# Performance work log

Hardware: AMD Instinct MI355X
Metric: run time of the kernel (lower is better)

Reference implementation:

```python
import jax, jax.numpy as jnp
import numpy as np

B = 64        # graphs per batch
NPG = 512     # nodes per graph (batch = repeat(arange(B), NPG))
D = 128       # hidden_dim = input_dim
L = 3         # GCN layers
K = 16        # NTN tensors
BINS = 16     # histogram bins


def _prep_edges(ei, N, dtype):
    # GCNConv normalization: add self-loops, deg on targets, sym norm
    loop = jnp.arange(N)
    src = jnp.concatenate([ei[0], loop])
    dst = jnp.concatenate([ei[1], loop])
    deg = jnp.zeros((N,), dtype).at[dst].add(1.0)
    dinv = jnp.where(deg > 0, jax.lax.rsqrt(deg), 0.0)
    norm = (dinv[src] * dinv[dst])[:, None]
    return src, dst, norm


def _encode(x, src, dst, norm, gcn_w, gcn_b, bn_g, bn_b, bn_m, bn_v):
    # eval-mode BatchNorm (running stats), dropout = identity
    for l in range(L):
        h = x @ gcn_w[l].T                     # [N, D]
        x = jnp.zeros_like(h).at[dst].add(norm * h[src]) + gcn_b[l]
        x = (x - bn_m[l]) * jax.lax.rsqrt(bn_v[l] + 1e-5) * bn_g[l] + bn_b[l]
        x = jax.nn.relu(x)
    return x


def _attention_pool(emb, ctx_w, ctx_b, att_w, att_b):
    t = jnp.tanh(emb @ ctx_w.T + ctx_b)        # [N, D]
    s = (t @ att_w + att_b).reshape(B, NPG, 1)
    e = emb.reshape(B, NPG, D)
    w = jax.nn.softmax(s, axis=1)              # per-graph softmax
    return (w * e).sum(axis=1)                 # [B, D]


def _histogram(e1, e2):
    n1 = (e1 / jnp.maximum(jnp.linalg.norm(e1, axis=-1, keepdims=True), 1e-8)).reshape(B, NPG, D)
    n2 = (e2 / jnp.maximum(jnp.linalg.norm(e2, axis=-1, keepdims=True), 1e-8)).reshape(B, NPG, D)
    sims = jnp.einsum('bnd,bmd->bnm', n1, n2)  # [B, n, n] cosine sims in [-1,1]
    bi = jnp.clip(jnp.floor((sims + 1.0) * (BINS / 2.0)), 0, BINS - 1).astype(jnp.int32)
    flat = (jnp.arange(B, dtype=jnp.int32)[:, None] * BINS + bi.reshape(B, -1)).reshape(-1)
    hist = jax.ops.segment_sum(jnp.ones(flat.shape, jnp.float32), flat,
                               num_segments=B * BINS).reshape(B, BINS)
    return hist / (hist.sum(axis=1, keepdims=True) + 1e-8)


def _ntn(g1, g2, T, tb, w1, b1, w2, b2, w3, b3):
    tp = jnp.einsum('bd,kde,be->bk', g1, T, g2) + tb   # bilinear products
    h = jax.nn.relu(tp @ w1.T + b1)
    h = jax.nn.relu(h @ w2.T + b2)
    return jax.nn.sigmoid(h @ w3.T + b3)               # [B, 1]


def _forward(x1, x2, edge_index1, edge_index2,
             gcn_w, gcn_b, bn_gamma, bn_beta, bn_mean, bn_var,
             ctx_w, ctx_b, att_w, att_b,
             ntn_T, ntn_bias, ntn_w1, ntn_b1, ntn_w2, ntn_b2, ntn_w3, ntn_b3,
             hist_w1, hist_b1, hist_w2, hist_b2,
             fus_w1, fus_b1, fus_w2, fus_b2):
    N = x1.shape[0]
    s1, d1, n1 = _prep_edges(edge_index1, N, x1.dtype)
    s2, d2, n2 = _prep_edges(edge_index2, N, x2.dtype)
    e1 = _encode(x1, s1, d1, n1, gcn_w, gcn_b, bn_gamma, bn_beta, bn_mean, bn_var)
    e2 = _encode(x2, s2, d2, n2, gcn_w, gcn_b, bn_gamma, bn_beta, bn_mean, bn_var)
    g1 = _attention_pool(e1, ctx_w, ctx_b, att_w, att_b)
    g2 = _attention_pool(e2, ctx_w, ctx_b, att_w, att_b)
    ntn_sim = _ntn(g1, g2, ntn_T, ntn_bias, ntn_w1, ntn_b1, ntn_w2, ntn_b2, ntn_w3, ntn_b3)
    hist = _histogram(e1, e2)
    hemb = jax.nn.relu(hist @ hist_w1.T + hist_b1) @ hist_w2.T + hist_b2
    comb = jnp.concatenate([ntn_sim, hemb], axis=1)    # [B, 17]
    h = jax.nn.relu(comb @ fus_w1.T + fus_b1)
    return jax.nn.sigmoid(h @ fus_w2.T + fus_b2)       # [B, 1]


def setup_inputs() -> dict:
    key = jax.random.key(0)
    ks = jax.random.split(key, 32)
    N = B * NPG
    E = 16 * N
    sc = 0.05
    inp = {
        'x1': jax.random.normal(ks[0], (N, D), jnp.float32),
        'x2': jax.random.normal(ks[1], (N, D), jnp.float32),
        'edge_index1': jax.random.randint(ks[2], (2, E), 0, N),
        'edge_index2': jax.random.randint(ks[3], (2, E), 0, N),
        'batch1': jnp.repeat(jnp.arange(B), NPG),
        'batch2': jnp.repeat(jnp.arange(B), NPG),
        'gcn_w': jax.random.normal(ks[4], (L, D, D), jnp.float32) * sc,
        'gcn_b': jax.random.normal(ks[5], (L, D), jnp.float32) * sc,
        'bn_gamma': jnp.ones((L, D), jnp.float32),
        'bn_beta': jnp.zeros((L, D), jnp.float32),
        'bn_mean': jnp.zeros((L, D), jnp.float32),
        'bn_var': jnp.ones((L, D), jnp.float32),
        'ctx_w': jax.random.normal(ks[6], (D, D), jnp.float32) * sc,
        'ctx_b': jax.random.normal(ks[7], (D,), jnp.float32) * sc,
        'att_w': jax.random.normal(ks[8], (D,), jnp.float32) * sc,
        'att_b': jax.random.normal(ks[9], (1,), jnp.float32) * sc,
        'ntn_T': jax.random.normal(ks[10], (K, D, D), jnp.float32) * 0.02,
        'ntn_bias': jax.random.normal(ks[11], (K,), jnp.float32) * sc,
        'ntn_w1': jax.random.normal(ks[12], (32, K), jnp.float32) * 0.2,
        'ntn_b1': jax.random.normal(ks[13], (32,), jnp.float32) * sc,
        'ntn_w2': jax.random.normal(ks[14], (16, 32), jnp.float32) * 0.15,
        'ntn_b2': jax.random.normal(ks[15], (16,), jnp.float32) * sc,
        'ntn_w3': jax.random.normal(ks[16], (1, 16), jnp.float32) * 0.2,
        'ntn_b3': jax.random.normal(ks[17], (1,), jnp.float32) * sc,
        'hist_w1': jax.random.normal(ks[18], (32, BINS), jnp.float32) * 0.2,
        'hist_b1': jax.random.normal(ks[19], (32,), jnp.float32) * sc,
        'hist_w2': jax.random.normal(ks[20], (16, 32), jnp.float32) * 0.15,
        'hist_b2': jax.random.normal(ks[21], (16,), jnp.float32) * sc,
        'fus_w1': jax.random.normal(ks[22], (8, 17), jnp.float32) * 0.2,
        'fus_b1': jax.random.normal(ks[23], (8,), jnp.float32) * sc,
        'fus_w2': jax.random.normal(ks[24], (1, 8), jnp.float32) * 0.3,
        'fus_b2': jax.random.normal(ks[25], (1,), jnp.float32) * sc,
    }
    return inp


def reference(x1, x2, edge_index1, edge_index2, batch1, batch2,
              gcn_w, gcn_b, bn_gamma, bn_beta, bn_mean, bn_var,
              ctx_w, ctx_b, att_w, att_b,
              ntn_T, ntn_bias, ntn_w1, ntn_b1, ntn_w2, ntn_b2, ntn_w3, ntn_b3,
              hist_w1, hist_b1, hist_w2, hist_b2,
              fus_w1, fus_b1, fus_w2, fus_b2):
    # batch1/batch2 encode 64 equal-sized graphs (repeat(arange(B), NPG));
    # the per-graph loops of the torch code become dense [B, NPG, D] ops.
    return _forward(x1, x2, edge_index1, edge_index2,
                    gcn_w, gcn_b, bn_gamma, bn_beta, bn_mean, bn_var,
                    ctx_w, ctx_b, att_w, att_b,
                    ntn_T, ntn_bias, ntn_w1, ntn_b1, ntn_w2, ntn_b2, ntn_w3, ntn_b3,
                    hist_w1, hist_b1, hist_w2, hist_b2,
                    fus_w1, fus_b1, fus_w2, fus_b2)
```

## Files before the change

kernel.cpp:

```cpp
#include <hip/hip_runtime.h>
#include <math.h>

#define NN 32768
#define BB 64
#define NPG 512
#define DD 128
#define LL 3
#define EE 524288
#define NBINS 16
#define KNTN 16
#define NND (NN*DD)
#define NBKT 128
#define BCAP 10240

typedef unsigned short ushort_t;
typedef __attribute__((ext_vector_type(8))) short short8;
typedef __attribute__((ext_vector_type(4))) float f32x4;

__device__ __forceinline__ ushort_t f2bf(float f) {
    unsigned u = __builtin_bit_cast(unsigned, f);
    u += 0x7FFFu + ((u >> 16) & 1u);
    return (ushort_t)(u >> 16);
}
__device__ __forceinline__ float bf2f(ushort_t h) {
    unsigned u = ((unsigned)h) << 16;
    return __builtin_bit_cast(float, u);
}
__device__ __forceinline__ unsigned pack2(float a, float b) {
    return (unsigned)f2bf(a) | ((unsigned)f2bf(b) << 16);
}
__device__ __forceinline__ float lo16(unsigned u) { return __builtin_bit_cast(float, u << 16); }
__device__ __forceinline__ float hi16(unsigned u) { return __builtin_bit_cast(float, u & 0xffff0000u); }

__global__ __launch_bounds__(256) void k_prep(const float* __restrict__ gw,
                                              const float* __restrict__ cw,
                                              const float* __restrict__ gcn_b,
                                              const float* __restrict__ bn_g,
                                              const float* __restrict__ bn_b,
                                              const float* __restrict__ bn_m,
                                              const float* __restrict__ bn_v,
                                              ushort_t* __restrict__ wbf,
                                              float* __restrict__ bnsc,
                                              float* __restrict__ bnsh,
                                              int* __restrict__ bcur,
                                              float* __restrict__ hist) {
    int b = blockIdx.x, t = threadIdx.x;
    if (b < 64) {
        int i = b * 256 + t;
        const float4 v = (i < 3 * DD * DD / 4) ? ((const float4*)gw)[i]
                                               : ((const float4*)cw)[i - 3 * DD * DD / 4];
        uint2 o;
        o.x = pack2(v.x, v.y);
        o.y = pack2(v.z, v.w);
        ((uint2*)wbf)[i] = o;
    } else {
        if (t < NBKT) bcur[t] = 0;
        for (int i = t; i < BB * NBINS; i += 256) hist[i] = 0.f;
        if (t < DD) {
            #pragma unroll
            for (int l = 0; l < LL; l++) {
                int c = l * DD + t;
                float sc = bn_g[c] * rsqrtf(bn_v[c] + 1e-5f);
                bnsc[c] = sc;
                bnsh[c] = (gcn_b[c] - bn_m[c]) * sc + bn_b[c];
            }
        }
    }
}

__global__ __launch_bounds__(256) void k_bucket(const int* __restrict__ ei1,
                                                const int* __restrict__ ei2,
                                                int* __restrict__ bcur,
                                                unsigned* __restrict__ ibuf) {
    __shared__ int cnt[NBKT], off[NBKT], gb[NBKT];
    __shared__ unsigned stage[2048];
    int t = threadIdx.x;
    int blk = blockIdx.x;
    const int* ei = (blk < 256) ? ei1 : ei2;
    int ebase = (blk & 255) * 2048;
    int addn = (blk < 256) ? 0 : NN;
    for (int i = t; i < NBKT; i += 256) cnt[i] = 0;
    __syncthreads();
    unsigned pk[8]; int rk[8];
    #pragma unroll
    for (int k = 0; k < 8; k++) {
        int e = ebase + t + k * 256;
        int s = ei[e] + addn;
        int d = ei[EE + e] + addn;
        pk[k] = (unsigned)s | ((unsigned)d << 16);
    }
    #pragma unroll
    for (int k = 0; k < 8; k++) {
        int bk = pk[k] >> 25;
        rk[k] = atomicAdd(&cnt[bk], 1);
    }
    __syncthreads();
    if (t < NBKT) off[t] = cnt[t];
    __syncthreads();
    for (int o = 1; o < NBKT; o <<= 1) {
        int v = 0;
        if (t < NBKT && t >= o) v = off[t - o];
        __syncthreads();
        if (t < NBKT) off[t] += v;
        __syncthreads();
    }
    #pragma unroll
    for (int k = 0; k < 8; k++) {
        int bk = pk[k] >> 25;
        stage[off[bk] - cnt[bk] + rk[k]] = pk[k];
    }
    if (t < NBKT) {
        int c = cnt[t];
        gb[t] = c > 0 ? atomicAdd(&bcur[t], c) : 0;
    }
    __syncthreads();
    #pragma unroll
    for (int k = 0; k < 8; k++) {
        int idx = t + k * 256;
        unsigned p = stage[idx];
        int bk = p >> 25;
        int pos = idx - (off[bk] - cnt[bk]);
        ibuf[(size_t)bk * BCAP + gb[bk] + pos] = p;
    }
}

__global__ __launch_bounds__(256) void k_bcsr(const unsigned* __restrict__ ibuf,
                                              const int* __restrict__ bcur,
                                              int* __restrict__ deg,
                                              float* __restrict__ dinv,
                                              int* __restrict__ rowstart,
                                              ushort_t* __restrict__ esrc) {
    __shared__ int cnt[512];
    __shared__ int ps[256];
    __shared__ int lcur[512];
    int bk = blockIdx.x, t = threadIdx.x;
    for (int i = t; i < 512; i += 256) cnt[i] = 0;
    __syncthreads();
    int n = bcur[bk];
    const unsigned* buf = ibuf + (size_t)bk * BCAP;
    for (int i = t; i < n; i += 256) {
        int dl = (buf[i] >> 16) & 511;
        atomicAdd(&cnt[dl], 1);
    }
    __syncthreads();
    int c0 = cnt[2 * t], c1 = cnt[2 * t + 1];
    ps[t] = c0 + c1;
    __syncthreads();
    for (int o = 1; o < 256; o <<= 1) {
        int v = (t >= o) ? ps[t - o] : 0;
        __syncthreads();
        ps[t] += v;
        __syncthreads();
    }
    int excl = (t == 0) ? 0 : ps[t - 1];
    int base = bk * BCAP;
    int g0 = bk * 512 + 2 * t, g1 = g0 + 1;
    deg[g0] = c0; deg[g1] = c1;
    dinv[g0] = rsqrtf((float)c0 + 1.0f);
    dinv[g1] = rsqrtf((float)c1 + 1.0f);
    int r0 = base + excl, r1 = base + excl + c0;
    rowstart[g0] = r0;
    rowstart[g1] = r1;
    lcur[2 * t] = r0;
    lcur[2 * t + 1] = r1;
    __syncthreads();
    for (int i = t; i < n; i += 256) {
        unsigned p = buf[i];
        int dl = (p >> 16) & 511;
        int slot = atomicAdd(&lcur[dl], 1);
        esrc[slot] = (ushort_t)(p & 0xffffu);
    }
}

template<int EPI, int XF>
__global__ __launch_bounds__(256) void k_mgemm(const ushort_t* __restrict__ X,
                                               const float* __restrict__ Xf1,
                                               const float* __restrict__ Xf2,
                                               const ushort_t* __restrict__ Wb,
                                               const float* __restrict__ bias,
                                               ushort_t* __restrict__ Out,
                                               const float* __restrict__ aw,
                                               const float* __restrict__ ab,
                                               float* __restrict__ Sout,
                                               const float* __restrict__ dscale) {
    __shared__ __align__(16) ushort_t wlds[128 * 128];
    int t = threadIdx.x;
    {
        int r = t >> 1, h = t & 1;
        const uint4* src = (const uint4*)(Wb + (size_t)r * DD + h * 64);
        #pragma unroll
        for (int i = 0; i < 8; i++) {
            int co = h * 128 + i * 16;
            int sw = co ^ ((r & 7) << 4);
            *(uint4*)&wlds[r * DD + (sw >> 1)] = src[i];
        }
    }
    __syncthreads();
    int w = t >> 6, l = t & 63;
    int rw = blockIdx.x * 128 + w * 32;
    int lr = l & 15, lg = l >> 4;
    f32x4 acc[2][8];
    #pragma unroll
    for (int g = 0; g < 2; g++)
        #pragma unroll
        for (int c = 0; c < 8; c++) acc[g][c] = (f32x4){0.f, 0.f, 0.f, 0.f};
    const ushort_t* xrow0 = X + (size_t)(rw + lr) * DD + lg * 8;
    const ushort_t* xrow1 = xrow0 + (size_t)16 * DD;
    const float* xf0 = nullptr;
    if (XF) {
        const float* xb = (rw < NN) ? Xf1 : (Xf2 - (size_t)NN * DD);
        xf0 = xb + (size_t)(rw + lr) * DD + lg * 8;
    }
    int swl = (lr & 7) << 4;
    for (int kt = 0; kt < 4; kt++) {
        short8 a0, a1;
        if (XF) {
            float4 va = *(const float4*)(xf0 + kt * 32);
            float4 vb = *(const float4*)(xf0 + kt * 32 + 4);
            float4 vc = *(const float4*)(xf0 + (size_t)16 * DD + kt * 32);
            float4 vd = *(const float4*)(xf0 + (size_t)16 * DD + kt * 32 + 4);
            a0[0] = (short)f2bf(va.x); a0[1] = (short)f2bf(va.y);
            a0[2] = (short)f2bf(va.z); a0[3] = (short)f2bf(va.w);
            a0[4] = (short)f2bf(vb.x); a0[5] = (short)f2bf(vb.y);
            a0[6] = (short)f2bf(vb.z); a0[7] = (short)f2bf(vb.w);
            a1[0] = (short)f2bf(vc.x); a1[1] = (short)f2bf(vc.y);
            a1[2] = (short)f2bf(vc.z); a1[3] = (short)f2bf(vc.w);
            a1[4] = (short)f2bf(vd.x); a1[5] = (short)f2bf(vd.y);
            a1[6] = (short)f2bf(vd.z); a1[7] = (short)f2bf(vd.w);
        } else {
            a0 = *(const short8*)(xrow0 + kt * 32);
            a1 = *(const short8*)(xrow1 + kt * 32);
        }
        int colsw = (kt * 64 + lg * 16) ^ swl;
        #pragma unroll
        for (int c = 0; c < 8; c++) {
            int row = c * 16 + lr;
            short8 b = *(const short8*)&wlds[row * DD + (colsw >> 1)];
            acc[0][c] = __builtin_amdgcn_mfma_f32_16x16x32_bf16(a0, b, acc[0][c], 0, 0, 0);
            acc[1][c] = __builtin_amdgcn_mfma_f32_16x16x32_bf16(a1, b, acc[1][c], 0, 0, 0);
        }
    }
    if (EPI == 0) {
        float ds[2][4];
        #pragma unroll
        for (int g = 0; g < 2; g++)
            #pragma unroll
            for (int q = 0; q < 4; q++) ds[g][q] = dscale[rw + g * 16 + lg * 4 + q];
        #pragma unroll
        for (int g = 0; g < 2; g++)
            #pragma unroll
            for (int c = 0; c < 8; c++) {
                int col = c * 16 + lr;
                #pragma unroll
                for (int q = 0; q < 4; q++)
                    Out[(size_t)(rw + g * 16 + lg * 4 + q) * DD + col] = f2bf(acc[g][c][q] * ds[g][q]);
            }
    } else {
        float rs[2][4] = {};
        #pragma unroll
        for (int c = 0; c < 8; c++) {
            int col = c * 16 + lr;
            float bv = bias[col], wv = aw[col];
            #pragma unroll
            for (int g = 0; g < 2; g++)
                #pragma unroll
                for (int q = 0; q < 4; q++)
                    rs[g][q] += tanhf(acc[g][c][q] + bv) * wv;
        }
        #pragma unroll
        for (int m = 1; m < 16; m <<= 1)
            #pragma unroll
            for (int g = 0; g < 2; g++)
                #pragma unroll
                for (int q = 0; q < 4; q++) rs[g][q] += __shfl_xor(rs[g][q], m);
        if (lr == 0) {
            float a0 = ab[0];
            #pragma unroll
            for (int g = 0; g < 2; g++)
                #pragma unroll
                for (int q = 0; q < 4; q++)
                    Sout[rw + g * 16 + lg * 4 + q] = rs[g][q] + a0;
        }
    }
}

#define GATHER(u, s) uint4 u = Hu4[(size_t)(s) * 16 + cl]
#define ACCUM(u) \
    a0 += lo16(u.x); a1 += hi16(u.x); a2 += lo16(u.y); a3 += hi16(u.y); \
    a4 += lo16(u.z); a5 += hi16(u.z); a6 += lo16(u.w); a7 += hi16(u.w)

template<int LAST>
__global__ __launch_bounds__(256) void k_agg(
    const ushort_t* __restrict__ Hs, const int* __restrict__ rowstart,
    const int* __restrict__ deg, const ushort_t* __restrict__ esrc,
    const float* __restrict__ dinv, const float* __restrict__ bnsc,
    const float* __restrict__ bnsh, ushort_t* __restrict__ A,
    ushort_t* __restrict__ Nrm) {
    int wid = (blockIdx.x * blockDim.x + threadIdx.x) >> 6;
    int l = threadIdx.x & 63;
    int q = l >> 4, cl = l & 15;
    int n = wid * 4 + q;
    const uint4* Hu4 = (const uint4*)Hs;
    int beg = rowstart[n];
    int end = beg + deg[n];
    float di = dinv[n];
    uint4 h = Hu4[(size_t)n * 16 + cl];
    float a0 = lo16(h.x), a1 = hi16(h.x), a2 = lo16(h.y), a3 = hi16(h.y);
    float a4 = lo16(h.z), a5 = hi16(h.z), a6 = lo16(h.w), a7 = hi16(h.w);
    int j = beg;
    for (; j + 8 <= end; j += 8) {
        unsigned s0 = esrc[j + 0], s1 = esrc[j + 1], s2 = esrc[j + 2], s3 = esrc[j + 3];
        unsigned s4 = esrc[j + 4], s5 = esrc[j + 5], s6 = esrc[j + 6], s7 = esrc[j + 7];
        GATHER(u0, s0); GATHER(u1, s1); GATHER(u2, s2); GATHER(u3, s3);
        GATHER(u4, s4); GATHER(u5, s5); GATHER(u6, s6); GATHER(u7, s7);
        ACCUM(u0); ACCUM(u1); ACCUM(u2); ACCUM(u3);
        ACCUM(u4); ACCUM(u5); ACCUM(u6); ACCUM(u7);
    }
    for (; j + 2 <= end; j += 2) {
        unsigned s0 = esrc[j], s1 = esrc[j + 1];
        GATHER(u0, s0); GATHER(u1, s1);
        ACCUM(u0); ACCUM(u1);
    }
    if (j < end) {
        unsigned s0 = esrc[j];
        GATHER(u0, s0);
        ACCUM(u0);
    }
    int c = cl * 8;
    float4 scA = *(const float4*)&bnsc[c], scB = *(const float4*)&bnsc[c + 4];
    float4 shA = *(const float4*)&bnsh[c], shB = *(const float4*)&bnsh[c + 4];
    float o0 = fmaf(a0 * di, scA.x, shA.x);
    float o1 = fmaf(a1 * di, scA.y, shA.y);
    float o2 = fmaf(a2 * di, scA.z, shA.z);
    float o3 = fmaf(a3 * di, scA.w, shA.w);
    float o4 = fmaf(a4 * di, scB.x, shB.x);
    float o5 = fmaf(a5 * di, scB.y, shB.y);
    float o6 = fmaf(a6 * di, scB.z, shB.z);
    float o7 = fmaf(a7 * di, scB.w, shB.w);
    uint4 av;
    av.x = pack2(fmaxf(o0, 0.f), fmaxf(o1, 0.f));
    av.y = pack2(fmaxf(o2, 0.f), fmaxf(o3, 0.f));
    av.z = pack2(fmaxf(o4, 0.f), fmaxf(o5, 0.f));
    av.w = pack2(fmaxf(o6, 0.f), fmaxf(o7, 0.f));
    ((uint4*)A)[(size_t)n * 16 + cl] = av;
    if (LAST) {
        float r0 = lo16(av.x), r1 = hi16(av.x), r2 = lo16(av.y), r3 = hi16(av.y);
        float r4 = lo16(av.z), r5 = hi16(av.z), r6 = lo16(av.w), r7 = hi16(av.w);
        float ss = ((r0 * r0 + r1 * r1) + (r2 * r2 + r3 * r3)) +
                   ((r4 * r4 + r5 * r5) + (r6 * r6 + r7 * r7));
        #pragma unroll
        for (int o = 8; o > 0; o >>= 1) ss += __shfl_xor(ss, o);
        float inv = 1.0f / fmaxf(sqrtf(ss), 1e-8f);
        uint4 nv;
        nv.x = pack2(r0 * inv, r1 * inv);
        nv.y = pack2(r2 * inv, r3 * inv);
        nv.z = pack2(r4 * inv, r5 * inv);
        nv.w = pack2(r6 * inv, r7 * inv);
        ((uint4*)Nrm)[(size_t)n * 16 + cl] = nv;
    }
}

__global__ __launch_bounds__(512) void k_pool2(const float* __restrict__ S,
                                               const ushort_t* __restrict__ Emb,
                                               float* __restrict__ G) {
    int b = blockIdx.x, t = threadIdx.x;
    __shared__ float red[512];
    __shared__ float w[512];
    __shared__ float red0[512], red1[512];
    float s = S[b * NPG + t];
    red[t] = s;
    __syncthreads();
    for (int o = 256; o > 0; o >>= 1) { if (t < o) red[t] = fmaxf(red[t], red[t + o]); __syncthreads(); }
    float m = red[0];
    __syncthreads();
    float e = expf(s - m);
    w[t] = e;
    red[t] = e;
    __syncthreads();
    for (int o = 256; o > 0; o >>= 1) { if (t < o) red[t] += red[t + o]; __syncthreads(); }
    float inv = 1.0f / red[0];
    int l = t & 63, ch = t >> 6;
    int nbase = b * NPG + ch * 64;
    float a0 = 0.f, a1 = 0.f;
    #pragma unroll 4
    for (int i = 0; i < 64; i++) {
        float wv = w[ch * 64 + i];
        unsigned u = ((const unsigned*)(Emb + (size_t)(nbase + i) * DD))[l];
        a0 += wv * lo16(u);
        a1 += wv * hi16(u);
    }
    red0[t] = a0; red1[t] = a1;
    __syncthreads();
    if (t < 64) {
        float s0 = 0.f, s1 = 0.f;
        #pragma unroll
        for (int c = 0; c < 8; c++) { s0 += red0[t + c * 64]; s1 += red1[t + c * 64]; }
        G[b * DD + 2 * t] = s0 * inv;
        G[b * DD + 2 * t + 1] = s1 * inv;
    }
}

__global__ __launch_bounds__(256) void k_hist(const ushort_t* __restrict__ N1,
                                              const ushort_t* __restrict__ N2,
                                              float* __restrict__ Hist) {
    __shared__ __align__(16) ushort_t blds[128 * 128];
    __shared__ int hl[256 * 17];
    __shared__ float hred[NBINS];
    int t = threadIdx.x, w = t >> 6, l = t & 63;
    int lr = l & 15, lg = l >> 4;
    int g = blockIdx.x >> 4, ti = (blockIdx.x >> 2) & 3, tj = blockIdx.x & 3;
    {
        int r = t >> 1, h = t & 1;
        const uint4* src = (const uint4*)(N2 + ((size_t)g * NPG + tj * 128 + r) * DD + h * 64);
        #pragma unroll
        for (int i = 0; i < 8; i++) {
            int co = h * 128 + i * 16;
            int sw = co ^ ((r & 7) << 4);
            *(uint4*)&blds[r * DD + (sw >> 1)] = src[i];
        }
    }
    #pragma unroll
    for (int i = t; i < 256 * 17; i += 256) hl[i] = 0;
    if (t < NBINS) hred[t] = 0.f;
    __syncthreads();

    const ushort_t* arow = N1 + ((size_t)g * NPG + ti * 128 + w * 32 + lr) * DD + lg * 8;
    f32x4 acc[2][8];
    #pragma unroll
    for (int r = 0; r < 2; r++)
        #pragma unroll
        for (int c = 0; c < 8; c++) acc[r][c] = (f32x4){0.f, 0.f, 0.f, 0.f};
    int swl = (lr & 7) << 4;
    for (int kt = 0; kt < 4; kt++) {
        short8 a0 = *(const short8*)(arow + kt * 32);
        short8 a1 = *(const short8*)(arow + (size_t)16 * DD + kt * 32);
        int colsw = (kt * 64 + lg * 16) ^ swl;
        #pragma unroll
        for (int c = 0; c < 8; c++) {
            int row = c * 16 + lr;
            short8 b = *(const short8*)&blds[row * DD + (colsw >> 1)];
            acc[0][c] = __builtin_amdgcn_mfma_f32_16x16x32_bf16(a0, b, acc[0][c], 0, 0, 0);
            acc[1][c] = __builtin_amdgcn_mfma_f32_16x16x32_bf16(a1, b, acc[1][c], 0, 0, 0);
        }
    }
    int base = t * 17;
    #pragma unroll
    for (int r = 0; r < 2; r++)
        #pragma unroll
        for (int c = 0; c < 8; c++)
            #pragma unroll
            for (int q = 0; q < 4; q++) {
                float sim = acc[r][c][q];
                float v = floorf((sim + 1.0f) * 8.0f);
                v = fminf(fmaxf(v, 0.f), 15.f);
                atomicAdd(&hl[base + (int)v], 1);
            }
    __syncthreads();
    int bin = t & 15, r0 = (t >> 4) * 16;
    int s = 0;
    #pragma unroll
    for (int r = 0; r < 16; r++) s += hl[(r0 + r) * 17 + bin];
    atomicAdd(&hred[bin], (float)s);
    __syncthreads();
    if (t < NBINS) atomicAdd(&Hist[g * NBINS + t], hred[t]);
}

__global__ __launch_bounds__(128) void k_ntn(const float* __restrict__ G1,
                                             const float* __restrict__ G2,
                                             const float* __restrict__ T,
                                             const float* __restrict__ tb,
                                             float* __restrict__ TP) {
    int b = blockIdx.x, k = blockIdx.y;
    int e = threadIdx.x;
    const float* Tk = T + (size_t)k * DD * DD;
    float g2e = G2[b * DD + e];
    float acc = 0.f;
    for (int d = 0; d < DD; d++) acc += G1[b * DD + d] * Tk[(size_t)d * DD + e];
    float val = acc * g2e;
    #pragma unroll
    for (int o = 32; o > 0; o >>= 1) val += __shfl_down(val, o);
    __shared__ float ps[2];
    if ((e & 63) == 0) ps[e >> 6] = val;
    __syncthreads();
    if (e == 0) TP[b * KNTN + k] = ps[0] + ps[1] + tb[k];
}

__global__ __launch_bounds__(256) void k_final(const float* __restrict__ TP, const float* __restrict__ Hist,
                        const float* nw1, const float* nb1, const float* nw2, const float* nb2,
                        const float* nw3, const float* nb3,
                        const float* hw1, const float* hb1, const float* hw2, const float* hb2,
                        const float* fw1, const float* fb1, const float* fw2, const float* fb2,
                        float* __restrict__ out) {
    __shared__ float sTP[BB * 16], sHist[BB * 16];
    __shared__ float snw1[512], snw2[512], shw1[512], shw2[512];
    __shared__ float snw3[16], snb1[32], snb2[16], shb1[32], shb2[16];
    __shared__ float sfw1[136], sfb1[8], sfw2[8], sscal[2];
    int t = threadIdx.x;
    for (int i = t; i < BB * 16; i += 256) { sTP[i] = TP[i]; sHist[i] = Hist[i]; }
    for (int i = t; i < 512; i += 256) {
        snw1[i] = nw1[i]; snw2[i] = nw2[i]; shw1[i] = hw1[i]; shw2[i] = hw2[i];
    }
    if (t < 136) sfw1[t] = fw1[t];
    if (t < 32) { snb1[t] = nb1[t]; shb1[t] = hb1[t]; }
    if (t < 16) { snb2[t] = nb2[t]; shb2[t] = hb2[t]; snw3[t] = nw3[t]; }
    if (t < 8) { sfb1[t] = fb1[t]; sfw2[t] = fw2[t]; }
    if (t == 0) { sscal[0] = nb3[0]; sscal[1] = fb2[0]; }
    __syncthreads();
    if (t >= BB) return;
    int b = t;
    float h1[32];
    #pragma unroll
    for (int i = 0; i < 32; i++) {
        float a = snb1[i];
        for (int k = 0; k < 16; k++) a += sTP[b * 16 + k] * snw1[i * 16 + k];
        h1[i] = fmaxf(a, 0.f);
    }
    float h2[16];
    #pragma unroll
    for (int j = 0; j < 16; j++) {
        float a = snb2[j];
        for (int i = 0; i < 32; i++) a += h1[i] * snw2[j * 32 + i];
        h2[j] = fmaxf(a, 0.f);
    }
    float nt = sscal[0];
    for (int j = 0; j < 16; j++) nt += h2[j] * snw3[j];
    nt = 1.f / (1.f + expf(-nt));
    float hh[16]; float sum = 0.f;
    for (int k = 0; k < 16; k++) { hh[k] = sHist[b * 16 + k]; sum += hh[k]; }
    float inv = 1.f / (sum + 1e-8f);
    for (int k = 0; k < 16; k++) hh[k] *= inv;
    float g1v[32];
    #pragma unroll
    for (int i = 0; i < 32; i++) {
        float a = shb1[i];
        for (int k = 0; k < 16; k++) a += hh[k] * shw1[i * 16 + k];
        g1v[i] = fmaxf(a, 0.f);
    }
    float hemb[16];
    #pragma unroll
    for (int j = 0; j < 16; j++) {
        float a = shb2[j];
        for (int i = 0; i < 32; i++) a += g1v[i] * shw2[j * 32 + i];
        hemb[j] = a;
    }
    float comb[17];
    comb[0] = nt;
    for (int j = 0; j < 16; j++) comb[1 + j] = hemb[j];
    float f1[8];
    #pragma unroll
    for (int i = 0; i < 8; i++) {
        float a = sfb1[i];
        for (int j = 0; j < 17; j++) a += comb[j] * sfw1[i * 17 + j];
        f1[i] = fmaxf(a, 0.f);
    }
    float o = sscal[1];
    for (int i = 0; i < 8; i++) o += f1[i] * sfw2[i];
    out[b] = 1.f / (1.f + expf(-o));
}

extern "C" void kernel_launch(void* const* d_in, const int* in_sizes, int n_in,
                              void* d_out, int out_size, void* d_ws, size_t ws_size,
                              hipStream_t stream) {
    const float* x1    = (const float*)d_in[0];
    const float* x2    = (const float*)d_in[1];
    const int*   ei1   = (const int*)d_in[2];
    const int*   ei2   = (const int*)d_in[3];
    const float* gcn_w = (const float*)d_in[6];
    const float* gcn_b = (const float*)d_in[7];
    const float* bn_g  = (const float*)d_in[8];
    const float* bn_b  = (const float*)d_in[9];
    const float* bn_m  = (const float*)d_in[10];
    const float* bn_v  = (const float*)d_in[11];
    const float* ctx_w = (const float*)d_in[12];
    const float* ctx_b = (const float*)d_in[13];
    const float* att_w = (const float*)d_in[14];
    const float* att_b = (const float*)d_in[15];
    const float* ntn_T = (const float*)d_in[16];
    const float* ntn_b = (const float*)d_in[17];
    const float* nw1 = (const float*)d_in[18];
    const float* nb1 = (const float*)d_in[19];
    const float* nw2 = (const float*)d_in[20];
    const float* nb2 = (const float*)d_in[21];
    const float* nw3 = (const float*)d_in[22];
    const float* nb3 = (const float*)d_in[23];
    const float* hw1 = (const float*)d_in[24];
    const float* hb1 = (const float*)d_in[25];
    const float* hw2 = (const float*)d_in[26];
    const float* hb2 = (const float*)d_in[27];
    const float* fw1 = (const float*)d_in[28];
    const float* fb1 = (const float*)d_in[29];
    const float* fw2 = (const float*)d_in[30];
    const float* fb2 = (const float*)d_in[31];
    float* out = (float*)d_out;

    ushort_t* Xbf = (ushort_t*)d_ws;
    ushort_t* Abf = Xbf + 2 * (size_t)NND;
    ushort_t* Hbf = Abf + 2 * (size_t)NND;
    ushort_t* wbf = Hbf + 2 * (size_t)NND;
    float* dinv = (float*)(wbf + 4 * DD * DD);
    float* S    = dinv + 2 * NN;
    float* G    = S + 2 * NN;
    float* hist = G + 2 * BB * DD;
    float* tp   = hist + BB * NBINS;
    float* bnsc = tp + BB * KNTN;
    float* bnsh = bnsc + LL * DD;
    int* degi  = (int*)(bnsh + LL * DD);
    int* rowst = degi + 2 * NN;
    int* bcur  = rowst + 2 * NN;
    ushort_t* esrc = (ushort_t*)(bcur + NBKT);
    unsigned* ibuf = (unsigned*)(esrc + (size_t)NBKT * BCAP);

    k_prep<<<65, 256, 0, stream>>>(gcn_w, ctx_w, gcn_b, bn_g, bn_b, bn_m, bn_v,
                                   wbf, bnsc, bnsh, bcur, hist);
    k_bucket<<<2 * EE / 2048, 256, 0, stream>>>(ei1, ei2, bcur, ibuf);
    k_bcsr<<<NBKT, 256, 0, stream>>>(ibuf, bcur, degi, dinv, rowst, esrc);

    for (int l = 0; l < LL; l++) {
        if (l == 0)
            k_mgemm<0, 1><<<2 * NN / 128, 256, 0, stream>>>(nullptr, x1, x2,
                                                            wbf, nullptr, Hbf,
                                                            nullptr, nullptr, nullptr, dinv);
        else
            k_mgemm<0, 0><<<2 * NN / 128, 256, 0, stream>>>(Abf, nullptr, nullptr,
                                                            wbf + (size_t)l * DD * DD,
                                                            nullptr, Hbf, nullptr, nullptr, nullptr, dinv);
        if (l < LL - 1)
            k_agg<0><<<2 * NN / 16, 256, 0, stream>>>(Hbf, rowst, degi, esrc, dinv,
                                                      bnsc + l * DD, bnsh + l * DD, Abf, nullptr);
        else
            k_agg<1><<<2 * NN / 16, 256, 0, stream>>>(Hbf, rowst, degi, esrc, dinv,
                                                      bnsc + l * DD, bnsh + l * DD, Abf, Xbf);
    }
    k_mgemm<2, 0><<<2 * NN / 128, 256, 0, stream>>>(Abf, nullptr, nullptr,
                                                    wbf + 3 * DD * DD, ctx_b,
                                                    nullptr, att_w, att_b, S, nullptr);
    k_pool2<<<2 * BB, 512, 0, stream>>>(S, Abf, G);
    k_hist<<<BB * 16, 256, 0, stream>>>(Xbf, Xbf + NND, hist);
    k_ntn<<<dim3(BB, KNTN), 128, 0, stream>>>(G, G + BB * DD, ntn_T, ntn_b, tp);
    k_final<<<1, 256, 0, stream>>>(tp, hist, nw1, nb1, nw2, nb2, nw3, nb3,
                                   hw1, hb1, hw2, hb2, fw1, fb1, fw2, fb2, out);
}
```

Baseline: 232.3 us.

## Replace global bucket atomics with per-block segments, fold prep, stage edge indices in LDS

The prep kernel is merged into the bucketing kernel as extra blocks. Bucketing now writes each block's edges into fixed per-(bucket,block) segments with counts, which drops the prefix scan, staging and global atomic cursors. The CSR build walks those segments. Aggregation preloads a block's edge source indices into shared memory, and the histogram writes per-tile partials that the final kernel reduces instead of using global atomics. The risks are segment overflow if any block sends more than 56 edges to one bucket, serial per-thread segment loops in the CSR build, and an LDS overflow if a 16-node block has more than 2048 edges.

New measurement: 216.3 us. -6.9%, faster.

```diff
diff --git a/kernel.cpp b/kernel.cpp
--- a/kernel.cpp
+++ b/kernel.cpp
@@ -11,7 +11,8 @@
 #define KNTN 16
 #define NND (NN*DD)
 #define NBKT 128
-#define BCAP 10240
+#define BSEG 56
+#define BCAPE 10240
 
 typedef unsigned short ushort_t;
 typedef __attribute__((ext_vector_type(8))) short short8;
@@ -32,31 +33,32 @@
 __device__ __forceinline__ float lo16(unsigned u) { return __builtin_bit_cast(float, u << 16); }
 __device__ __forceinline__ float hi16(unsigned u) { return __builtin_bit_cast(float, u & 0xffff0000u); }
 
-__global__ __launch_bounds__(256) void k_prep(const float* __restrict__ gw,
-                                              const float* __restrict__ cw,
-                                              const float* __restrict__ gcn_b,
-                                              const float* __restrict__ bn_g,
-                                              const float* __restrict__ bn_b,
-                                              const float* __restrict__ bn_m,
-                                              const float* __restrict__ bn_v,
-                                              ushort_t* __restrict__ wbf,
-                                              float* __restrict__ bnsc,
-                                              float* __restrict__ bnsh,
-                                              int* __restrict__ bcur,
-                                              float* __restrict__ hist) {
-    int b = blockIdx.x, t = threadIdx.x;
-    if (b < 64) {
-        int i = b * 256 + t;
-        const float4 v = (i < 3 * DD * DD / 4) ? ((const float4*)gw)[i]
-                                               : ((const float4*)cw)[i - 3 * DD * DD / 4];
-        uint2 o;
-        o.x = pack2(v.x, v.y);
-        o.y = pack2(v.z, v.w);
-        ((uint2*)wbf)[i] = o;
-    } else {
-        if (t < NBKT) bcur[t] = 0;
-        for (int i = t; i < BB * NBINS; i += 256) hist[i] = 0.f;
-        if (t < DD) {
+__global__ __launch_bounds__(256) void k_bucket(const int* __restrict__ ei1,
+                                                const int* __restrict__ ei2,
+                                                unsigned* __restrict__ ibuf,
+                                                int* __restrict__ bcnt,
+                                                const float* __restrict__ gw,
+                                                const float* __restrict__ cw,
+                                                ushort_t* __restrict__ wbf,
+                                                const float* __restrict__ gcn_b,
+                                                const float* __restrict__ bn_g,
+                                                const float* __restrict__ bn_b,
+                                                const float* __restrict__ bn_m,
+                                                const float* __restrict__ bn_v,
+                                                float* __restrict__ bnsc,
+                                                float* __restrict__ bnsh) {
+    int t = threadIdx.x;
+    int blk = blockIdx.x;
+    if (blk >= 512) {
+        if (blk < 576) {
+            int i = (blk - 512) * 256 + t;
+            const float4 v = (i < 3 * DD * DD / 4) ? ((const float4*)gw)[i]
+                                                   : ((const float4*)cw)[i - 3 * DD * DD / 4];
+            uint2 o;
+            o.x = pack2(v.x, v.y);
+            o.y = pack2(v.z, v.w);
+            ((uint2*)wbf)[i] = o;
+        } else if (t < DD) {
             #pragma unroll
             for (int l = 0; l < LL; l++) {
                 int c = l * DD + t;
@@ -65,67 +67,30 @@
                 bnsh[c] = (gcn_b[c] - bn_m[c]) * sc + bn_b[c];
             }
         }
-    }
-}
-
-__global__ __launch_bounds__(256) void k_bucket(const int* __restrict__ ei1,
-                                                const int* __restrict__ ei2,
-                                                int* __restrict__ bcur,
-                                                unsigned* __restrict__ ibuf) {
-    __shared__ int cnt[NBKT], off[NBKT], gb[NBKT];
-    __shared__ unsigned stage[2048];
-    int t = threadIdx.x;
-    int blk = blockIdx.x;
+        return;
+    }
+    __shared__ int cnt[NBKT];
     const int* ei = (blk < 256) ? ei1 : ei2;
     int ebase = (blk & 255) * 2048;
     int addn = (blk < 256) ? 0 : NN;
     for (int i = t; i < NBKT; i += 256) cnt[i] = 0;
     __syncthreads();
-    unsigned pk[8]; int rk[8];
     #pragma unroll
     for (int k = 0; k < 8; k++) {
         int e = ebase + t + k * 256;
         int s = ei[e] + addn;
         int d = ei[EE + e] + addn;
-        pk[k] = (unsigned)s | ((unsigned)d << 16);
-    }
-    #pragma unroll
-    for (int k = 0; k < 8; k++) {
-        int bk = pk[k] >> 25;
-        rk[k] = atomicAdd(&cnt[bk], 1);
-    }
-    __syncthreads();
-    if (t < NBKT) off[t] = cnt[t];
-    __syncthreads();
-    for (int o = 1; o < NBKT; o <<= 1) {
-        int v = 0;
-        if (t < NBKT && t >= o) v = off[t - o];
-        __syncthreads();
-        if (t < NBKT) off[t] += v;
-        __syncthreads();
-    }
-    #pragma unroll
-    for (int k = 0; k < 8; k++) {
-        int bk = pk[k] >> 25;
-        stage[off[bk] - cnt[bk] + rk[k]] = pk[k];
-    }
-    if (t < NBKT) {
-        int c = cnt[t];
-        gb[t] = c > 0 ? atomicAdd(&bcur[t], c) : 0;
-    }
-    __syncthreads();
-    #pragma unroll
-    for (int k = 0; k < 8; k++) {
-        int idx = t + k * 256;
-        unsigned p = stage[idx];
-        int bk = p >> 25;
-        int pos = idx - (off[bk] - cnt[bk]);
-        ibuf[(size_t)bk * BCAP + gb[bk] + pos] = p;
-    }
+        unsigned p = (unsigned)s | ((unsigned)d << 16);
+        int bk = (unsigned)d >> 9;
+        int rk = atomicAdd(&cnt[bk], 1);
+        ibuf[(size_t)(bk * 512 + blk) * BSEG + rk] = p;
+    }
+    __syncthreads();
+    if (t < NBKT) bcnt[t * 512 + blk] = cnt[t];
 }
 
 __global__ __launch_bounds__(256) void k_bcsr(const unsigned* __restrict__ ibuf,
-                                              const int* __restrict__ bcur,
+                                              const int* __restrict__ bcnt,
                                               int* __restrict__ deg,
                                               float* __restrict__ dinv,
                                               int* __restrict__ rowstart,
@@ -136,11 +101,13 @@
     int bk = blockIdx.x, t = threadIdx.x;
     for (int i = t; i < 512; i += 256) cnt[i] = 0;
     __syncthreads();
-    int n = bcur[bk];
-    const unsigned* buf = ibuf + (size_t)bk * BCAP;
-    for (int i = t; i < n; i += 256) {
-        int dl = (buf[i] >> 16) & 511;
-        atomicAdd(&cnt[dl], 1);
+    for (int b = t; b < 512; b += 256) {
+        int n = bcnt[bk * 512 + b];
+        const unsigned* seg = ibuf + (size_t)(bk * 512 + b) * BSEG;
+        for (int i = 0; i < n; i++) {
+            int dl = (seg[i] >> 16) & 511;
+            atomicAdd(&cnt[dl], 1);
+        }
     }
     __syncthreads();
     int c0 = cnt[2 * t], c1 = cnt[2 * t + 1];
@@ -153,7 +120,7 @@
         __syncthreads();
     }
     int excl = (t == 0) ? 0 : ps[t - 1];
-    int base = bk * BCAP;
+    int base = bk * BCAPE;
     int g0 = bk * 512 + 2 * t, g1 = g0 + 1;
     deg[g0] = c0; deg[g1] = c1;
     dinv[g0] = rsqrtf((float)c0 + 1.0f);
@@ -164,11 +131,15 @@
     lcur[2 * t] = r0;
     lcur[2 * t + 1] = r1;
     __syncthreads();
-    for (int i = t; i < n; i += 256) {
-        unsigned p = buf[i];
-        int dl = (p >> 16) & 511;
-        int slot = atomicAdd(&lcur[dl], 1);
-        esrc[slot] = (ushort_t)(p & 0xffffu);
+    for (int b = t; b < 512; b += 256) {
+        int n = bcnt[bk * 512 + b];
+        const unsigned* seg = ibuf + (size_t)(bk * 512 + b) * BSEG;
+        for (int i = 0; i < n; i++) {
+            unsigned p = seg[i];
+            int dl = (p >> 16) & 511;
+            int slot = atomicAdd(&lcur[dl], 1);
+            esrc[slot] = (ushort_t)(p & 0xffffu);
+        }
     }
 }
 
@@ -296,12 +267,17 @@
     const float* __restrict__ dinv, const float* __restrict__ bnsc,
     const float* __restrict__ bnsh, ushort_t* __restrict__ A,
     ushort_t* __restrict__ Nrm) {
-    int wid = (blockIdx.x * blockDim.x + threadIdx.x) >> 6;
+    __shared__ ushort_t sidx[2048];
+    int nb0 = blockIdx.x * 16;
+    int blockBeg = rowstart[nb0];
+    int blockCnt = rowstart[nb0 + 15] + deg[nb0 + 15] - blockBeg;
+    for (int i = threadIdx.x; i < blockCnt; i += 256) sidx[i] = esrc[blockBeg + i];
+    __syncthreads();
     int l = threadIdx.x & 63;
     int q = l >> 4, cl = l & 15;
-    int n = wid * 4 + q;
+    int n = nb0 + (threadIdx.x >> 6) * 4 + q;
     const uint4* Hu4 = (const uint4*)Hs;
-    int beg = rowstart[n];
+    int beg = rowstart[n] - blockBeg;
     int end = beg + deg[n];
     float di = dinv[n];
     uint4 h = Hu4[(size_t)n * 16 + cl];
@@ -309,20 +285,20 @@
     float a4 = lo16(h.z), a5 = hi16(h.z), a6 = lo16(h.w), a7 = hi16(h.w);
     int j = beg;
     for (; j + 8 <= end; j += 8) {
-        unsigned s0 = esrc[j + 0], s1 = esrc[j + 1], s2 = esrc[j + 2], s3 = esrc[j + 3];
-        unsigned s4 = esrc[j + 4], s5 = esrc[j + 5], s6 = esrc[j + 6], s7 = esrc[j + 7];
+        unsigned s0 = sidx[j + 0], s1 = sidx[j + 1], s2 = sidx[j + 2], s3 = sidx[j + 3];
+        unsigned s4 = sidx[j + 4], s5 = sidx[j + 5], s6 = sidx[j + 6], s7 = sidx[j + 7];
         GATHER(u0, s0); GATHER(u1, s1); GATHER(u2, s2); GATHER(u3, s3);
         GATHER(u4, s4); GATHER(u5, s5); GATHER(u6, s6); GATHER(u7, s7);
         ACCUM(u0); ACCUM(u1); ACCUM(u2); ACCUM(u3);
         ACCUM(u4); ACCUM(u5); ACCUM(u6); ACCUM(u7);
     }
     for (; j + 2 <= end; j += 2) {
-        unsigned s0 = esrc[j], s1 = esrc[j + 1];
+        unsigned s0 = sidx[j], s1 = sidx[j + 1];
         GATHER(u0, s0); GATHER(u1, s1);
         ACCUM(u0); ACCUM(u1);
     }
     if (j < end) {
-        unsigned s0 = esrc[j];
+        unsigned s0 = sidx[j];
         GATHER(u0, s0);
         ACCUM(u0);
     }
@@ -402,7 +378,7 @@
 
 __global__ __launch_bounds__(256) void k_hist(const ushort_t* __restrict__ N1,
                                               const ushort_t* __restrict__ N2,
-                                              float* __restrict__ Hist) {
+                                              float* __restrict__ Histp) {
     __shared__ __align__(16) ushort_t blds[128 * 128];
     __shared__ int hl[256 * 17];
     __shared__ float hred[NBINS];
@@ -462,7 +438,7 @@
     for (int r = 0; r < 16; r++) s += hl[(r0 + r) * 17 + bin];
     atomicAdd(&hred[bin], (float)s);
     __syncthreads();
-    if (t < NBINS) atomicAdd(&Hist[g * NBINS + t], hred[t]);
+    if (t < NBINS) Histp[((size_t)g * 16 + (ti * 4 + tj)) * NBINS + t] = hred[t];
 }
 
 __global__ __launch_bounds__(128) void k_ntn(const float* __restrict__ G1,
@@ -485,7 +461,7 @@
     if (e == 0) TP[b * KNTN + k] = ps[0] + ps[1] + tb[k];
 }
 
-__global__ __launch_bounds__(256) void k_final(const float* __restrict__ TP, const float* __restrict__ Hist,
+__global__ __launch_bounds__(256) void k_final(const float* __restrict__ TP, const float* __restrict__ Histp,
                         const float* nw1, const float* nb1, const float* nw2, const float* nb2,
                         const float* nw3, const float* nb3,
                         const float* hw1, const float* hb1, const float* hw2, const float* hb2,
@@ -496,7 +472,14 @@
     __shared__ float snw3[16], snb1[32], snb2[16], shb1[32], shb2[16];
     __shared__ float sfw1[136], sfb1[8], sfw2[8], sscal[2];
     int t = threadIdx.x;
-    for (int i = t; i < BB * 16; i += 256) { sTP[i] = TP[i]; sHist[i] = Hist[i]; }
+    for (int i = t; i < BB * 16; i += 256) {
+        sTP[i] = TP[i];
+        int b = i >> 4, bin = i & 15;
+        float s = 0.f;
+        #pragma unroll
+        for (int tile = 0; tile < 16; tile++) s += Histp[((size_t)b * 16 + tile) * NBINS + bin];
+        sHist[i] = s;
+    }
     for (int i = t; i < 512; i += 256) {
         snw1[i] = nw1[i]; snw2[i] = nw2[i]; shw1[i] = hw1[i]; shw2[i] = hw2[i];
     }
@@ -600,20 +583,19 @@
     float* dinv = (float*)(wbf + 4 * DD * DD);
     float* S    = dinv + 2 * NN;
     float* G    = S + 2 * NN;
-    float* hist = G + 2 * BB * DD;
-    float* tp   = hist + BB * NBINS;
+    float* histp = G + 2 * BB * DD;
+    float* tp   = histp + BB * 16 * NBINS;
     float* bnsc = tp + BB * KNTN;
     float* bnsh = bnsc + LL * DD;
     int* degi  = (int*)(bnsh + LL * DD);
     int* rowst = degi + 2 * NN;
-    int* bcur  = rowst + 2 * NN;
-    ushort_t* esrc = (ushort_t*)(bcur + NBKT);
-    unsigned* ibuf = (unsigned*)(esrc + (size_t)NBKT * BCAP);
-
-    k_prep<<<65, 256, 0, stream>>>(gcn_w, ctx_w, gcn_b, bn_g, bn_b, bn_m, bn_v,
-                                   wbf, bnsc, bnsh, bcur, hist);
-    k_bucket<<<2 * EE / 2048, 256, 0, stream>>>(ei1, ei2, bcur, ibuf);
-    k_bcsr<<<NBKT, 256, 0, stream>>>(ibuf, bcur, degi, dinv, rowst, esrc);
+    int* bcnt  = rowst + 2 * NN;
+    ushort_t* esrc = (ushort_t*)(bcnt + NBKT * 512);
+    unsigned* ibuf = (unsigned*)(esrc + (size_t)NBKT * BCAPE);
+
+    k_bucket<<<577, 256, 0, stream>>>(ei1, ei2, ibuf, bcnt, gcn_w, ctx_w, wbf,
+                                      gcn_b, bn_g, bn_b, bn_m, bn_v, bnsc, bnsh);
+    k_bcsr<<<NBKT, 256, 0, stream>>>(ibuf, bcnt, degi, dinv, rowst, esrc);
 
     for (int l = 0; l < LL; l++) {
         if (l == 0)
@@ -635,8 +617,8 @@
                                                     wbf + 3 * DD * DD, ctx_b,
                                                     nullptr, att_w, att_b, S, nullptr);
     k_pool2<<<2 * BB, 512, 0, stream>>>(S, Abf, G);
-    k_hist<<<BB * 16, 256, 0, stream>>>(Xbf, Xbf + NND, hist);
+    k_hist<<<BB * 16, 256, 0, stream>>>(Xbf, Xbf + NND, histp);
     k_ntn<<<dim3(BB, KNTN), 128, 0, stream>>>(G, G + BB * DD, ntn_T, ntn_b, tp);
-    k_final<<<1, 256, 0, stream>>>(tp, hist, nw1, nb1, nw2, nb2, nw3, nb3,
+    k_final<<<1, 256, 0, stream>>>(tp, histp, nw1, nb1, nw2, nb2, nw3, nb3,
                                    hw1, hb1, hw2, hb2, fw1, fb1, fw2, fb2, out);
 }
```
